# Performance work log

Hardware: AMD Instinct MI355X
Metric: run time of the kernel (lower is better)

Reference implementation:

```python
import jax, jax.numpy as jnp
import numpy as np

TOP_K = 2  # num_experts_per_tok


def setup_inputs() -> dict:
    key = jax.random.key(0)
    k1, k2, k3, k4, k5 = jax.random.split(key, 5)
    B, S, D, F, E = 2, 1024, 1024, 2048, 8
    return {
        "x": jax.random.normal(k1, (B, S, D), dtype=jnp.float32),
        "router_kernel_DE": jax.random.normal(k2, (D, E), dtype=jnp.float32) * 0.02,
        "kernel_gating_EDF": jax.random.normal(k3, (E, D, F), dtype=jnp.float32) * 0.02,
        "kernel_up_EDF": jax.random.normal(k4, (E, D, F), dtype=jnp.float32) * 0.02,
        "kernel_down_EFD": jax.random.normal(k5, (E, F, D), dtype=jnp.float32) * 0.02,
    }


def reference(x, router_kernel_DE, kernel_gating_EDF, kernel_up_EDF, kernel_down_EFD):
    E = router_kernel_DE.shape[-1]
    x = x.astype(jnp.float32)
    # --- Router ---
    logits_BSE = jnp.einsum('BSD,DE->BSE', x, router_kernel_DE)
    probs_BSE = jax.nn.softmax(logits_BSE.astype(jnp.float32), axis=-1)
    weights_BSK, indices_BSK = jax.lax.top_k(probs_BSE, TOP_K)
    norm_weights_BSK = jax.nn.softmax(weights_BSK, axis=-1)
    # scatter top-k weights into dense [B,S,E]
    one_hot_BSKE = jax.nn.one_hot(indices_BSK, num_classes=E, dtype=x.dtype)
    full_weights_BSE = jnp.sum(one_hot_BSKE * norm_weights_BSK[..., None], axis=2)
    # --- Dense-over-all-experts MoE forward ---
    gating_BSEF = jnp.einsum('BSD,EDF->BSEF', x, kernel_gating_EDF)
    act_BSEF = jax.nn.silu(gating_BSEF)
    up_BSEF = jnp.einsum('BSD,EDF->BSEF', x, kernel_up_EDF)
    fuse_BSEF = act_BSEF * up_BSEF
    down_BSED = jnp.einsum('BSEF,EFD->BSED', fuse_BSEF, kernel_down_EFD)
    out_BSD = jnp.einsum('BSED,BSE->BSD', down_BSED, full_weights_BSE)
    return out_BSD.astype(jnp.float32)
```

## Files before the change

kernel.cpp:

```cpp
#include <hip/hip_runtime.h>
#include <hip/hip_bf16.h>
#include <stdint.h>

#define T_TOK 2048
#define DIM 1024
#define FDIM 2048
#define NEXP 8
#define NSLOT 4096

typedef short bf16x8 __attribute__((ext_vector_type(8)));
typedef unsigned short u16x8 __attribute__((ext_vector_type(8)));
typedef float f32x4 __attribute__((ext_vector_type(4)));

__device__ __forceinline__ unsigned short f2bf(float f) {
  union { float f; unsigned int u; } v; v.f = f;
  unsigned int r = v.u + 0x7FFFu + ((v.u >> 16) & 1u);
  return (unsigned short)(r >> 16);
}

__device__ __forceinline__ float bf2f(unsigned short x) {
  union { unsigned int u; float f; } v; v.u = ((unsigned int)x) << 16;
  return v.f;
}

__device__ __forceinline__ void gld_lds16(const void* g, void* l) {
  __builtin_amdgcn_global_load_lds(
      (const __attribute__((address_space(1))) unsigned int*)g,
      (__attribute__((address_space(3))) unsigned int*)l, 16, 0, 0);
}

__global__ void router_kernel(const float* __restrict__ x, const float* __restrict__ rk,
                              int* __restrict__ counts, int* __restrict__ tok_e,
                              float* __restrict__ tok_w, unsigned short* __restrict__ xb) {
  int w = threadIdx.x >> 6, lane = threadIdx.x & 63;
  int t = blockIdx.x * 4 + w;
  float acc[NEXP];
#pragma unroll
  for (int e = 0; e < NEXP; ++e) acc[e] = 0.f;
  const float4* xr = (const float4*)(x + (size_t)t * DIM);
#pragma unroll
  for (int i = 0; i < 4; ++i) {
    float4 xv = xr[i * 64 + lane];
    uint2 pk;
    pk.x = ((unsigned)f2bf(xv.y) << 16) | f2bf(xv.x);
    pk.y = ((unsigned)f2bf(xv.w) << 16) | f2bf(xv.z);
    *(uint2*)(xb + (size_t)t * DIM + (i * 64 + lane) * 4) = pk;
    int d0 = (i * 64 + lane) * 4;
#pragma unroll
    for (int j = 0; j < 4; ++j) {
      const float4* rr = (const float4*)(rk + (size_t)(d0 + j) * NEXP);
      float4 r0 = rr[0], r1 = rr[1];
      float xs = (j == 0) ? xv.x : (j == 1) ? xv.y : (j == 2) ? xv.z : xv.w;
      acc[0] += xs * r0.x; acc[1] += xs * r0.y; acc[2] += xs * r0.z; acc[3] += xs * r0.w;
      acc[4] += xs * r1.x; acc[5] += xs * r1.y; acc[6] += xs * r1.z; acc[7] += xs * r1.w;
    }
  }
#pragma unroll
  for (int off = 32; off > 0; off >>= 1) {
#pragma unroll
    for (int e = 0; e < NEXP; ++e) acc[e] += __shfl_xor(acc[e], off, 64);
  }
  if (lane == 0) {
    float m = acc[0];
    for (int e = 1; e < NEXP; ++e) m = fmaxf(m, acc[e]);
    float p[NEXP], s = 0.f;
    for (int e = 0; e < NEXP; ++e) { p[e] = expf(acc[e] - m); s += p[e]; }
    float inv = 1.f / s;
    for (int e = 0; e < NEXP; ++e) p[e] *= inv;
    int i1 = 0;
    for (int e = 1; e < NEXP; ++e) if (p[e] > p[i1]) i1 = e;
    int i2 = (i1 == 0) ? 1 : 0;
    for (int e = 0; e < NEXP; ++e) if (e != i1 && p[e] > p[i2]) i2 = e;
    float e1 = expf(p[i1]), e2 = expf(p[i2]);
    float winv = 1.f / (e1 + e2);
    tok_e[t * 2] = i1; tok_e[t * 2 + 1] = i2;
    tok_w[t * 2] = e1 * winv; tok_w[t * 2 + 1] = e2 * winv;
    atomicAdd(&counts[i1], 1); atomicAdd(&counts[i2], 1);
  }
}

__global__ void assign_kernel(const int* __restrict__ tok_e, const float* __restrict__ tok_w,
                              const int* __restrict__ counts, int* __restrict__ cursor,
                              int* __restrict__ slot_token, float* __restrict__ slot_weight,
                              int* __restrict__ tok_slot) {
  int t = blockIdx.x * 256 + threadIdx.x;
  if (t >= T_TOK) return;
#pragma unroll
  for (int k = 0; k < 2; ++k) {
    int e = tok_e[t * 2 + k];
    int off = 0;
#pragma unroll
    for (int j = 0; j < NEXP; ++j) off += (j < e) ? counts[j] : 0;
    int pos = atomicAdd(&cursor[e], 1);
    int slot = off + pos;
    slot_token[slot] = t;
    slot_weight[slot] = tok_w[t * 2 + k];
    tok_slot[t * 2 + k] = slot;
  }
}

__global__ void transpose_all(const float* __restrict__ wg_f, const float* __restrict__ wu_f,
                              const float* __restrict__ wd_f, unsigned short* __restrict__ wgt,
                              unsigned short* __restrict__ wut, unsigned short* __restrict__ wdt) {
  __shared__ float lds[64][65];
  int bid = blockIdx.x, e = blockIdx.y;
  const float* in;
  unsigned short* out;
  int R, C, rb, cb;
  if (bid < 1024) {
    in = (bid < 512) ? wg_f : wu_f;
    out = (bid < 512) ? wgt : wut;
    int id = bid & 511;
    R = DIM; C = FDIM;
    cb = (id & 31) * 64; rb = (id >> 5) * 64;
  } else {
    in = wd_f; out = wdt;
    int id = bid - 1024;
    R = FDIM; C = DIM;
    cb = (id & 15) * 64; rb = (id >> 4) * 64;
  }
  size_t base = (size_t)e * (size_t)R * (size_t)C;
  int tid = threadIdx.x;
  int col4 = (tid & 15) * 4, row = tid >> 4;
#pragma unroll
  for (int it = 0; it < 4; ++it) {
    int r = row + it * 16;
    float4 v = *(const float4*)(in + base + (size_t)(rb + r) * C + cb + col4);
    lds[col4 + 0][r] = v.x; lds[col4 + 1][r] = v.y;
    lds[col4 + 2][r] = v.z; lds[col4 + 3][r] = v.w;
  }
  __syncthreads();
  int r8 = (tid & 7) * 8, c = tid >> 3;
#pragma unroll
  for (int it = 0; it < 2; ++it) {
    int cc = c + it * 32;
    uint4 v;
    v.x = ((unsigned)f2bf(lds[cc][r8 + 1]) << 16) | f2bf(lds[cc][r8 + 0]);
    v.y = ((unsigned)f2bf(lds[cc][r8 + 3]) << 16) | f2bf(lds[cc][r8 + 2]);
    v.z = ((unsigned)f2bf(lds[cc][r8 + 5]) << 16) | f2bf(lds[cc][r8 + 4]);
    v.w = ((unsigned)f2bf(lds[cc][r8 + 7]) << 16) | f2bf(lds[cc][r8 + 6]);
    *(uint4*)(out + base + (size_t)(cb + cc) * R + rb + r8) = v;
  }
}

__device__ __forceinline__ bool tile_decode(const int* counts, int ys, int& e, int& mt,
                                            int& off, int& cnt) {
  mt = ys; off = 0;
  for (e = 0; e < NEXP; ++e) {
    cnt = counts[e];
    int ntl = (cnt + 127) >> 7;
    if (mt < ntl) return true;
    mt -= ntl; off += cnt;
  }
  return false;
}

__global__ __launch_bounds__(256) void gemm_gateup(
    const unsigned short* __restrict__ xb, const unsigned short* __restrict__ wg,
    const unsigned short* __restrict__ wu, const int* __restrict__ counts,
    const int* __restrict__ slot_token, unsigned short* __restrict__ fuse) {
  int e, mt, off, cnt;
  if (!tile_decode(counts, blockIdx.y, e, mt, off, cnt)) return;
  int nt = blockIdx.x;
  __shared__ unsigned short Al[128 * 64];
  __shared__ unsigned short Bgl[2][64 * 64];
  __shared__ unsigned short Bul[2][64 * 64];
  int tid = threadIdx.x, w = tid >> 6, lane = tid & 63;
  int csrc = ((lane & 7) ^ (lane >> 3)) * 8;
  unsigned aoff[4];
  unsigned boff[2];
#pragma unroll
  for (int ii = 0; ii < 4; ++ii) {
    int r = (w * 4 + ii) * 8 + (lane >> 3);
    int row = mt * 128 + r;
    int tok = (row < cnt) ? slot_token[off + row] : 0;
    aoff[ii] = (unsigned)(tok * DIM + csrc);
  }
#pragma unroll
  for (int ii = 0; ii < 2; ++ii) {
    int r = (w * 2 + ii) * 8 + (lane >> 3);
    boff[ii] = (unsigned)((e * FDIM + nt * 64 + r) * DIM + csrc);
  }
  f32x4 accg[4][2] = {};
  f32x4 accu[4][2] = {};
  int wr = (w >> 1) * 64, wc = (w & 1) * 32;
  int swz = (lane & 7) << 3;
  int kof0 = ((lane >> 4) * 8) ^ swz;
  int kof1 = (32 + (lane >> 4) * 8) ^ swz;

  auto stage_A = [&](int k0) {
#pragma unroll
    for (int ii = 0; ii < 4; ++ii)
      gld_lds16(xb + aoff[ii] + k0, &Al[(w * 4 + ii) * 512]);
  };
  auto stage_B = [&](int buf, int k0) {
#pragma unroll
    for (int ii = 0; ii < 2; ++ii) {
      gld_lds16(wg + boff[ii] + k0, &Bgl[buf][(w * 2 + ii) * 512]);
      gld_lds16(wu + boff[ii] + k0, &Bul[buf][(w * 2 + ii) * 512]);
    }
  };
  auto compute = [&](int buf) {
#pragma unroll
    for (int kk = 0; kk < 2; ++kk) {
      int kof = kk ? kof1 : kof0;
      bf16x8 af[4], bg[2], bu[2];
#pragma unroll
      for (int q = 0; q < 4; ++q)
        af[q] = *(const bf16x8*)&Al[(wr + q * 16 + (lane & 15)) * 64 + kof];
#pragma unroll
      for (int q = 0; q < 2; ++q) {
        bg[q] = *(const bf16x8*)&Bgl[buf][(wc + q * 16 + (lane & 15)) * 64 + kof];
        bu[q] = *(const bf16x8*)&Bul[buf][(wc + q * 16 + (lane & 15)) * 64 + kof];
      }
#pragma unroll
      for (int m4 = 0; m4 < 4; ++m4) {
#pragma unroll
        for (int n4 = 0; n4 < 2; ++n4) {
          accg[m4][n4] = __builtin_amdgcn_mfma_f32_16x16x32_bf16(af[m4], bg[n4], accg[m4][n4], 0, 0, 0);
          accu[m4][n4] = __builtin_amdgcn_mfma_f32_16x16x32_bf16(af[m4], bu[n4], accu[m4][n4], 0, 0, 0);
        }
      }
    }
  };

  stage_B(0, 0);
  stage_A(0);
  asm volatile("s_waitcnt vmcnt(0)" ::: "memory");
  __builtin_amdgcn_s_barrier();
  int cb = 0;
  for (int t = 0; t < 16; ++t) {
    if (t < 15) {
      stage_B(cb ^ 1, (t + 1) * 64);
      __builtin_amdgcn_sched_barrier(0);
      asm volatile("s_waitcnt vmcnt(4)" ::: "memory");
    } else {
      asm volatile("s_waitcnt vmcnt(0)" ::: "memory");
    }
    __builtin_amdgcn_s_barrier();
    __builtin_amdgcn_sched_barrier(0);
    compute(cb);
    __builtin_amdgcn_sched_barrier(0);
    __builtin_amdgcn_s_barrier();
    if (t < 15) stage_A((t + 1) * 64);
    cb ^= 1;
  }

#pragma unroll
  for (int m4 = 0; m4 < 4; ++m4) {
#pragma unroll
    for (int n4 = 0; n4 < 2; ++n4) {
      f32x4 g = accg[m4][n4], u = accu[m4][n4];
#pragma unroll
      for (int j = 0; j < 4; ++j) {
        int r = wr + m4 * 16 + (lane >> 4) * 4 + j;
        int row = mt * 128 + r;
        if (row < cnt) {
          float gv = g[j];
          float val = gv / (1.f + expf(-gv)) * u[j];
          int f = nt * 64 + wc + n4 * 16 + (lane & 15);
          fuse[(size_t)(off + row) * FDIM + f] = f2bf(val);
        }
      }
    }
  }
}

__global__ __launch_bounds__(256) void gemm_down(
    const unsigned short* __restrict__ fuse, const unsigned short* __restrict__ wd,
    const int* __restrict__ counts, const float* __restrict__ slot_weight,
    unsigned short* __restrict__ part4) {
  int e, mt, off, cnt;
  if (!tile_decode(counts, blockIdx.y, e, mt, off, cnt)) return;
  int nt = blockIdx.x;
  int z = blockIdx.z;
  int kbase = z * (FDIM / 4);
  __shared__ unsigned short Al[128 * 64];
  __shared__ unsigned short Bl[2][128 * 64];
  int tid = threadIdx.x, w = tid >> 6, lane = tid & 63;
  int csrc = ((lane & 7) ^ (lane >> 3)) * 8;
  unsigned aoff[4];
  unsigned boff[4];
#pragma unroll
  for (int ii = 0; ii < 4; ++ii) {
    int r = (w * 4 + ii) * 8 + (lane >> 3);
    int row = mt * 128 + r;
    int grow = (row < cnt) ? (off + row) : off;
    aoff[ii] = (unsigned)(grow * FDIM + kbase + csrc);
    boff[ii] = (unsigned)((e * DIM + nt * 128 + r) * FDIM + kbase + csrc);
  }
  f32x4 acc[4][4] = {};
  int wr = (w >> 1) * 64, wc = (w & 1) * 64;
  int swz = (lane & 7) << 3;
  int kof0 = ((lane >> 4) * 8) ^ swz;
  int kof1 = (32 + (lane >> 4) * 8) ^ swz;

  auto stage_A = [&](int k0) {
#pragma unroll
    for (int ii = 0; ii < 4; ++ii)
      gld_lds16(fuse + aoff[ii] + k0, &Al[(w * 4 + ii) * 512]);
  };
  auto stage_B = [&](int buf, int k0) {
#pragma unroll
    for (int ii = 0; ii < 4; ++ii)
      gld_lds16(wd + boff[ii] + k0, &Bl[buf][(w * 4 + ii) * 512]);
  };
  auto compute = [&](int buf) {
#pragma unroll
    for (int kk = 0; kk < 2; ++kk) {
      int kof = kk ? kof1 : kof0;
      bf16x8 af[4], bfr[4];
#pragma unroll
      for (int q = 0; q < 4; ++q) {
        af[q] = *(const bf16x8*)&Al[(wr + q * 16 + (lane & 15)) * 64 + kof];
        bfr[q] = *(const bf16x8*)&Bl[buf][(wc + q * 16 + (lane & 15)) * 64 + kof];
      }
#pragma unroll
      for (int m4 = 0; m4 < 4; ++m4) {
#pragma unroll
        for (int n4 = 0; n4 < 4; ++n4) {
          acc[m4][n4] = __builtin_amdgcn_mfma_f32_16x16x32_bf16(af[m4], bfr[n4], acc[m4][n4], 0, 0, 0);
        }
      }
    }
  };

  stage_B(0, 0);
  stage_A(0);
  asm volatile("s_waitcnt vmcnt(0)" ::: "memory");
  __builtin_amdgcn_s_barrier();
  int cb = 0;
  for (int t = 0; t < 8; ++t) {
    if (t < 7) {
      stage_B(cb ^ 1, (t + 1) * 64);
      __builtin_amdgcn_sched_barrier(0);
      asm volatile("s_waitcnt vmcnt(4)" ::: "memory");
    } else {
      asm volatile("s_waitcnt vmcnt(0)" ::: "memory");
    }
    __builtin_amdgcn_s_barrier();
    __builtin_amdgcn_sched_barrier(0);
    compute(cb);
    __builtin_amdgcn_sched_barrier(0);
    __builtin_amdgcn_s_barrier();
    if (t < 7) stage_A((t + 1) * 64);
    cb ^= 1;
  }

#pragma unroll
  for (int m4 = 0; m4 < 4; ++m4) {
#pragma unroll
    for (int j = 0; j < 4; ++j) {
      int r = wr + m4 * 16 + (lane >> 4) * 4 + j;
      int row = mt * 128 + r;
      if (row < cnt) {
        float wgt = slot_weight[off + row];
#pragma unroll
        for (int n4 = 0; n4 < 4; ++n4) {
          int d = nt * 128 + wc + n4 * 16 + (lane & 15);
          part4[((size_t)z * NSLOT + off + row) * DIM + d] = f2bf(acc[m4][n4][j] * wgt);
        }
      }
    }
  }
}

__global__ void combine_kernel(const unsigned short* __restrict__ part4,
                               const int* __restrict__ tok_slot, float* __restrict__ out) {
  int i = blockIdx.x * 256 + threadIdx.x;
  int t = i >> 7;
  int c = i & 127;
  int s0 = tok_slot[t * 2], s1 = tok_slot[t * 2 + 1];
  const u16x8* base = (const u16x8*)part4;
  float o[8];
#pragma unroll
  for (int j = 0; j < 8; ++j) o[j] = 0.f;
#pragma unroll
  for (int z = 0; z < 4; ++z) {
    u16x8 a = base[((size_t)z * NSLOT + s0) * (DIM / 8) + c];
    u16x8 b = base[((size_t)z * NSLOT + s1) * (DIM / 8) + c];
#pragma unroll
    for (int j = 0; j < 8; ++j) o[j] += bf2f(a[j]) + bf2f(b[j]);
  }
  float4* dst = (float4*)(out + (size_t)t * DIM + c * 8);
  dst[0] = make_float4(o[0], o[1], o[2], o[3]);
  dst[1] = make_float4(o[4], o[5], o[6], o[7]);
}

extern "C" void kernel_launch(void* const* d_in, const int* in_sizes, int n_in,
                              void* d_out, int out_size, void* d_ws, size_t ws_size,
                              hipStream_t stream) {
  (void)in_sizes; (void)n_in; (void)out_size;
  const float* x    = (const float*)d_in[0];
  const float* rk   = (const float*)d_in[1];
  const float* wg_f = (const float*)d_in[2];
  const float* wu_f = (const float*)d_in[3];
  const float* wd_f = (const float*)d_in[4];
  float* out = (float*)d_out;

  char* ws = (char*)d_ws;
  size_t o_xb   = 0;
  size_t o_wg   = o_xb + (size_t)T_TOK * DIM * 2;
  size_t o_wu   = o_wg + (size_t)NEXP * FDIM * DIM * 2;
  size_t o_wd   = o_wu + (size_t)NEXP * FDIM * DIM * 2;
  size_t o_fuse = o_wd + (size_t)NEXP * DIM * FDIM * 2;
  size_t o_meta = o_fuse + (size_t)NSLOT * FDIM * 2;
  size_t o_counts = o_meta;
  size_t o_cursor = o_counts + 32;
  size_t o_tok_e  = o_cursor + 32;
  size_t o_tok_w  = o_tok_e + (size_t)T_TOK * 2 * 4;
  size_t o_tok_s  = o_tok_w + (size_t)T_TOK * 2 * 4;
  size_t o_st     = o_tok_s + (size_t)T_TOK * 2 * 4;
  size_t o_sw     = o_st + (size_t)NSLOT * 4;
  size_t need     = o_sw + (size_t)NSLOT * 4;
  if (ws_size < need) return;

  unsigned short* xb    = (unsigned short*)(ws + o_xb);
  unsigned short* wgt   = (unsigned short*)(ws + o_wg);
  unsigned short* wut   = (unsigned short*)(ws + o_wu);
  unsigned short* wdt   = (unsigned short*)(ws + o_wd);
  unsigned short* fuse  = (unsigned short*)(ws + o_fuse);
  unsigned short* part4 = (unsigned short*)(ws + o_wg);
  int* counts          = (int*)(ws + o_counts);
  int* cursor          = (int*)(ws + o_cursor);
  int* tok_e           = (int*)(ws + o_tok_e);
  float* tok_w         = (float*)(ws + o_tok_w);
  int* tok_slot        = (int*)(ws + o_tok_s);
  int* slot_token      = (int*)(ws + o_st);
  float* slot_weight   = (float*)(ws + o_sw);

  hipMemsetAsync(ws + o_counts, 0, 64, stream);
  router_kernel<<<T_TOK / 4, 256, 0, stream>>>(x, rk, counts, tok_e, tok_w, xb);
  assign_kernel<<<T_TOK / 256, 256, 0, stream>>>(tok_e, tok_w, counts, cursor,
                                                 slot_token, slot_weight, tok_slot);
  transpose_all<<<dim3(1536, NEXP), 256, 0, stream>>>(wg_f, wu_f, wd_f, wgt, wut, wdt);
  gemm_gateup<<<dim3(FDIM / 64, 40, 1), 256, 0, stream>>>(xb, wgt, wut, counts,
                                                          slot_token, fuse);
  gemm_down<<<dim3(DIM / 128, 40, 4), 256, 0, stream>>>(fuse, wdt, counts,
                                                        slot_weight, part4);
  combine_kernel<<<(T_TOK * DIM / 8) / 256, 256, 0, stream>>>(part4, tok_slot, out);
}
```

Measured before the change: 243.6 us.

## Double-buffer A tile in gate/up GEMM and retile weight transpose to 128x32

The gate/up GEMM now double-buffers the activation tile alongside the weight tiles, so one combined stage prefetches the next K-slice while the current one is computed. This replaces the split A/B staging that needed two barriers per iteration. The weight transpose switches from 64x64 to 128x32 tiles, giving each output row 256-byte contiguous writes. It is also split into two launches, down-projection weights first, then gate/up. The costs are doubled LDS for the A tile, which may lower occupancy, and an extra kernel launch.

```diff
diff --git a/kernel.cpp b/kernel.cpp
--- a/kernel.cpp
+++ b/kernel.cpp
@@ -101,9 +101,10 @@
 
 __global__ void transpose_all(const float* __restrict__ wg_f, const float* __restrict__ wu_f,
                               const float* __restrict__ wd_f, unsigned short* __restrict__ wgt,
-                              unsigned short* __restrict__ wut, unsigned short* __restrict__ wdt) {
-  __shared__ float lds[64][65];
-  int bid = blockIdx.x, e = blockIdx.y;
+                              unsigned short* __restrict__ wut, unsigned short* __restrict__ wdt,
+                              int bid0) {
+  __shared__ float lds[32][129];
+  int bid = blockIdx.x + bid0, e = blockIdx.y;
   const float* in;
   unsigned short* out;
   int R, C, rb, cb;
@@ -112,28 +113,28 @@
     out = (bid < 512) ? wgt : wut;
     int id = bid & 511;
     R = DIM; C = FDIM;
-    cb = (id & 31) * 64; rb = (id >> 5) * 64;
+    cb = (id & 63) * 32; rb = (id >> 6) * 128;
   } else {
     in = wd_f; out = wdt;
     int id = bid - 1024;
     R = FDIM; C = DIM;
-    cb = (id & 15) * 64; rb = (id >> 4) * 64;
+    cb = (id & 31) * 32; rb = (id >> 5) * 128;
   }
   size_t base = (size_t)e * (size_t)R * (size_t)C;
   int tid = threadIdx.x;
-  int col4 = (tid & 15) * 4, row = tid >> 4;
+  int c4 = (tid & 7) * 4, row = tid >> 3;
 #pragma unroll
   for (int it = 0; it < 4; ++it) {
-    int r = row + it * 16;
-    float4 v = *(const float4*)(in + base + (size_t)(rb + r) * C + cb + col4);
-    lds[col4 + 0][r] = v.x; lds[col4 + 1][r] = v.y;
-    lds[col4 + 2][r] = v.z; lds[col4 + 3][r] = v.w;
+    int r = row + it * 32;
+    float4 v = *(const float4*)(in + base + (size_t)(rb + r) * C + cb + c4);
+    lds[c4 + 0][r] = v.x; lds[c4 + 1][r] = v.y;
+    lds[c4 + 2][r] = v.z; lds[c4 + 3][r] = v.w;
   }
   __syncthreads();
-  int r8 = (tid & 7) * 8, c = tid >> 3;
+  int r8 = (tid & 15) * 8, c = tid >> 4;
 #pragma unroll
   for (int it = 0; it < 2; ++it) {
-    int cc = c + it * 32;
+    int cc = c + it * 16;
     uint4 v;
     v.x = ((unsigned)f2bf(lds[cc][r8 + 1]) << 16) | f2bf(lds[cc][r8 + 0]);
     v.y = ((unsigned)f2bf(lds[cc][r8 + 3]) << 16) | f2bf(lds[cc][r8 + 2]);
@@ -162,7 +163,7 @@
   int e, mt, off, cnt;
   if (!tile_decode(counts, blockIdx.y, e, mt, off, cnt)) return;
   int nt = blockIdx.x;
-  __shared__ unsigned short Al[128 * 64];
+  __shared__ unsigned short Al[2][128 * 64];
   __shared__ unsigned short Bgl[2][64 * 64];
   __shared__ unsigned short Bul[2][64 * 64];
   int tid = threadIdx.x, w = tid >> 6, lane = tid & 63;
@@ -188,12 +189,10 @@
   int kof0 = ((lane >> 4) * 8) ^ swz;
   int kof1 = (32 + (lane >> 4) * 8) ^ swz;
 
-  auto stage_A = [&](int k0) {
+  auto stage = [&](int buf, int k0) {
 #pragma unroll
     for (int ii = 0; ii < 4; ++ii)
-      gld_lds16(xb + aoff[ii] + k0, &Al[(w * 4 + ii) * 512]);
-  };
-  auto stage_B = [&](int buf, int k0) {
+      gld_lds16(xb + aoff[ii] + k0, &Al[buf][(w * 4 + ii) * 512]);
 #pragma unroll
     for (int ii = 0; ii < 2; ++ii) {
       gld_lds16(wg + boff[ii] + k0, &Bgl[buf][(w * 2 + ii) * 512]);
@@ -207,7 +206,7 @@
       bf16x8 af[4], bg[2], bu[2];
 #pragma unroll
       for (int q = 0; q < 4; ++q)
-        af[q] = *(const bf16x8*)&Al[(wr + q * 16 + (lane & 15)) * 64 + kof];
+        af[q] = *(const bf16x8*)&Al[buf][(wr + q * 16 + (lane & 15)) * 64 + kof];
 #pragma unroll
       for (int q = 0; q < 2; ++q) {
         bg[q] = *(const bf16x8*)&Bgl[buf][(wc + q * 16 + (lane & 15)) * 64 + kof];
@@ -224,25 +223,17 @@
     }
   };
 
-  stage_B(0, 0);
-  stage_A(0);
+  stage(0, 0);
   asm volatile("s_waitcnt vmcnt(0)" ::: "memory");
   __builtin_amdgcn_s_barrier();
   int cb = 0;
-  for (int t = 0; t < 16; ++t) {
-    if (t < 15) {
-      stage_B(cb ^ 1, (t + 1) * 64);
-      __builtin_amdgcn_sched_barrier(0);
-      asm volatile("s_waitcnt vmcnt(4)" ::: "memory");
-    } else {
-      asm volatile("s_waitcnt vmcnt(0)" ::: "memory");
-    }
-    __builtin_amdgcn_s_barrier();
+  for (int k0 = 0; k0 < DIM; k0 += 64) {
+    if (k0 + 64 < DIM) stage(cb ^ 1, k0 + 64);
     __builtin_amdgcn_sched_barrier(0);
     compute(cb);
     __builtin_amdgcn_sched_barrier(0);
+    asm volatile("s_waitcnt vmcnt(0)" ::: "memory");
     __builtin_amdgcn_s_barrier();
-    if (t < 15) stage_A((t + 1) * 64);
     cb ^= 1;
   }
 
@@ -433,7 +424,8 @@
   router_kernel<<<T_TOK / 4, 256, 0, stream>>>(x, rk, counts, tok_e, tok_w, xb);
   assign_kernel<<<T_TOK / 256, 256, 0, stream>>>(tok_e, tok_w, counts, cursor,
                                                  slot_token, slot_weight, tok_slot);
-  transpose_all<<<dim3(1536, NEXP), 256, 0, stream>>>(wg_f, wu_f, wd_f, wgt, wut, wdt);
+  transpose_all<<<dim3(512, NEXP), 256, 0, stream>>>(wg_f, wu_f, wd_f, wgt, wut, wdt, 1024);
+  transpose_all<<<dim3(1024, NEXP), 256, 0, stream>>>(wg_f, wu_f, wd_f, wgt, wut, wdt, 0);
   gemm_gateup<<<dim3(FDIM / 64, 40, 1), 256, 0, stream>>>(xb, wgt, wut, counts,
                                                           slot_token, fuse);
   gemm_down<<<dim3(DIM / 128, 40, 4), 256, 0, stream>>>(fuse, wdt, counts,
```

New measurement: 245.6 us. Within noise of the previous version (+0.8%).
